# Performance work log

Measured on AMD Instinct MI355X. Metric: run time of the kernel, lower is better.

Reference implementation:

```python
import jax, jax.numpy as jnp
import numpy as np

B, S, D, H = 2, 2048, 2048, 16
HD = D // H  # head_dim = 128


def setup_inputs() -> dict:
    key = jax.random.key(0)
    ks = jax.random.split(key, 5)
    scale = 1.0 / np.sqrt(D)
    return {
        "x": jax.random.normal(ks[0], (B, S, D), dtype=jnp.float32),
        "wq": jax.random.normal(ks[1], (D, D), dtype=jnp.float32) * scale,
        "wk": jax.random.normal(ks[2], (D, D), dtype=jnp.float32) * scale,
        "wv": jax.random.normal(ks[3], (D, D), dtype=jnp.float32) * scale,
        "wo": jax.random.normal(ks[4], (D, D), dtype=jnp.float32) * scale,
        "bo": jnp.zeros((D,), dtype=jnp.float32),
    }


def reference(x, wq, wk, wv, wo, bo):
    b, s, _ = x.shape
    # torch Linear: y = x @ W.T ; then view(b,s,H,HD) and transpose to (b,H,s,HD)
    q = (x @ wq.T).reshape(b, s, H, HD).transpose(0, 2, 1, 3)
    k = (x @ wk.T).reshape(b, s, H, HD).transpose(0, 2, 1, 3)
    v = (x @ wv.T).reshape(b, s, H, HD).transpose(0, 2, 1, 3)
    scores = jnp.einsum("bhqd,bhkd->bhqk", q, k)
    causal = jnp.triu(jnp.ones((s, s), dtype=bool), k=1)  # True above diagonal
    scores = jnp.where(causal[None, None], -jnp.inf, scores)
    attn = jax.nn.softmax(scores / np.sqrt(HD), axis=-1)
    # dropout p=0.0 -> identity
    ctx = jnp.einsum("bhqk,bhkd->bhqd", attn, v)
    ctx = ctx.transpose(0, 2, 1, 3).reshape(b, s, D)
    return ctx @ wo.T + bo
```

## Files before the change

### kernel.cpp

```cpp
#include <hip/hip_runtime.h>
#include <math.h>

typedef __bf16 bf16_t;
typedef __bf16 bf16x8 __attribute__((ext_vector_type(8)));
typedef float f32x4 __attribute__((ext_vector_type(4)));
typedef float f32x16 __attribute__((ext_vector_type(16)));

__device__ __forceinline__ void gload_lds16(const bf16_t* g, bf16_t* l) {
    __builtin_amdgcn_global_load_lds((const __attribute__((address_space(1))) void*)g,
                                     (__attribute__((address_space(3))) void*)l, 16, 0, 0);
}

__global__ __launch_bounds__(256) void cvt_all(const float* __restrict__ x,
                                               const float* __restrict__ wq,
                                               const float* __restrict__ wk,
                                               const float* __restrict__ wv,
                                               const float* __restrict__ wo,
                                               bf16_t* __restrict__ dst) {
    int c = blockIdx.x * 256 + threadIdx.x;
    const float* src;
    size_t off;
    if (c < 1048576) { src = x; off = c; }
    else {
        int q = (c - 1048576) >> 19;
        src = (q == 0) ? wq : (q == 1) ? wk : (q == 2) ? wv : wo;
        off = (c - 1048576) & 524287;
    }
    const float4* p = (const float4*)src + off * 2;
    float4 a = p[0], b = p[1];
    union { bf16_t h[8]; uint4 u; } pk;
    pk.h[0] = (bf16_t)a.x; pk.h[1] = (bf16_t)a.y; pk.h[2] = (bf16_t)a.z; pk.h[3] = (bf16_t)a.w;
    pk.h[4] = (bf16_t)b.x; pk.h[5] = (bf16_t)b.y; pk.h[6] = (bf16_t)b.z; pk.h[7] = (bf16_t)b.w;
    ((uint4*)dst)[c] = pk.u;
}

template <int MODE, typename OutT>
__device__ __forceinline__ void gemm_core(bf16_t* __restrict__ AsB, bf16_t* __restrict__ BsB,
                                          const bf16_t* __restrict__ A,
                                          const bf16_t* __restrict__ Bm,
                                          const float* __restrict__ bias,
                                          OutT* __restrict__ C, bf16_t* __restrict__ Vt,
                                          int M, int N, int K, int bx, int by) {
    const int tid = threadIdx.x;
    const int w = tid >> 6, l = tid & 63;
    const int l16 = l & 15, lg = l >> 4;
    const int wr = w >> 1, wc = w & 1;
    const int m0 = bx * 256, n0 = by * 128;
    const int lsw = l16 & 7;

    f32x4 acc[4][4] = {};

    auto stageA = [&](int k0, int buf) {
#pragma unroll
        for (int j = 0; j < 4; ++j) {
            int c = tid + j * 512;
            int row = c >> 3;
            int kc = (c & 7) ^ (row & 7);
            gload_lds16(A + (size_t)(m0 + row) * K + k0 + kc * 8,
                        &AsB[buf * 16384 + (j * 512 + w * 64) * 8]);
        }
    };
    auto stageB = [&](int k0, int buf) {
#pragma unroll
        for (int j = 0; j < 2; ++j) {
            int c = tid + j * 512;
            int row = c >> 3;
            int kc = (c & 7) ^ (row & 7);
            gload_lds16(Bm + (size_t)(n0 + row) * K + k0 + kc * 8,
                        &BsB[buf * 8192 + (j * 512 + w * 64) * 8]);
        }
    };

    stageA(0, 0); stageB(0, 0);
    stageA(64, 1); stageB(64, 1);
    asm volatile("s_waitcnt vmcnt(6)" ::: "memory");
    __builtin_amdgcn_s_barrier();

    const int nt = K / 64;
    int cur = 0;
    for (int t = 0; t < nt; ++t) {
        int nxt = cur + 2; if (nxt >= 3) nxt -= 3;
        const bool pf = (t + 2 < nt);
        const int k2 = (t + 2) * 64;
        const bf16_t* Asc = &AsB[cur * 16384];
        const bf16_t* Bsc = &BsB[cur * 8192];

        if (pf) { stageA(k2, nxt); stageB(k2, nxt); }

        bf16x8 af[4][2], bfr[4][2];
#pragma unroll
        for (int mf = 0; mf < 4; ++mf)
#pragma unroll
            for (int ks = 0; ks < 2; ++ks) {
                int arow = wr * 64 + mf * 16 + l16;
                af[mf][ks] = *(const bf16x8*)&Asc[arow * 64 + (((ks << 2) | lg) ^ lsw) * 8];
            }
#pragma unroll
        for (int nf = 0; nf < 4; ++nf)
#pragma unroll
            for (int ks = 0; ks < 2; ++ks) {
                int brow = wc * 64 + nf * 16 + l16;
                bfr[nf][ks] = *(const bf16x8*)&Bsc[brow * 64 + (((ks << 2) | lg) ^ lsw) * 8];
            }
#pragma unroll
        for (int ks = 0; ks < 2; ++ks)
#pragma unroll
            for (int mf = 0; mf < 4; ++mf)
#pragma unroll
                for (int nf = 0; nf < 4; ++nf)
                    acc[mf][nf] = __builtin_amdgcn_mfma_f32_16x16x32_bf16(af[mf][ks], bfr[nf][ks], acc[mf][nf], 0, 0, 0);

        if (pf) asm volatile("s_waitcnt vmcnt(6)" ::: "memory");
        else    asm volatile("s_waitcnt vmcnt(0)" ::: "memory");
        __builtin_amdgcn_s_barrier();
        cur = (cur + 1 == 3) ? 0 : cur + 1;
    }

    if constexpr (MODE == 2) {
#pragma unroll
        for (int mf = 0; mf < 4; ++mf)
#pragma unroll
            for (int nf = 0; nf < 4; ++nf) {
                int col = n0 + wc * 64 + nf * 16 + l16;
                int hh = col >> 7, dh = col & 127;
                int rowbase = m0 + wr * 64 + mf * 16 + lg * 4;
                int bb = rowbase >> 11, s = rowbase & 2047;
                union { bf16_t h[4]; ushort4 u4; } pk;
#pragma unroll
                for (int r = 0; r < 4; ++r) pk.h[r] = (bf16_t)acc[mf][nf][r];
                *(ushort4*)&Vt[(((size_t)(bb * 16 + hh)) * 128 + dh) * 2048 + s] = pk.u4;
            }
    } else {
#pragma unroll
        for (int mf = 0; mf < 4; ++mf)
#pragma unroll
            for (int nf = 0; nf < 4; ++nf) {
                int col = n0 + wc * 64 + nf * 16 + l16;
                float bv = (MODE == 1) ? bias[col] : 0.f;
#pragma unroll
                for (int r = 0; r < 4; ++r) {
                    int row = m0 + wr * 64 + mf * 16 + lg * 4 + r;
                    C[(size_t)row * N + col] = (OutT)(acc[mf][nf][r] + bv);
                }
            }
    }
}

__global__ __launch_bounds__(512, 2) void gemm_qkv(const bf16_t* __restrict__ A,
                                                   const bf16_t* __restrict__ W0,
                                                   const bf16_t* __restrict__ W1,
                                                   const bf16_t* __restrict__ W2,
                                                   bf16_t* __restrict__ O0, bf16_t* __restrict__ O1,
                                                   bf16_t* __restrict__ Vt, int M, int N, int K) {
    __shared__ __align__(16) bf16_t As[3 * 256 * 64];
    __shared__ __align__(16) bf16_t Bs[3 * 128 * 64];
    int flat = blockIdx.x + 16 * (blockIdx.y + 16 * blockIdx.z);
    int idx = (flat & 7) * 96 + (flat >> 3);
    int bx = idx & 15, by = (idx >> 4) & 15, bz = idx >> 8;
    if (bz == 0)      gemm_core<0, bf16_t>(As, Bs, A, W0, nullptr, O0, nullptr, M, N, K, bx, by);
    else if (bz == 1) gemm_core<0, bf16_t>(As, Bs, A, W1, nullptr, O1, nullptr, M, N, K, bx, by);
    else              gemm_core<2, bf16_t>(As, Bs, A, W2, nullptr, (bf16_t*)nullptr, Vt, M, N, K, bx, by);
}

__global__ __launch_bounds__(512, 2) void gemm_bias_f32(const bf16_t* __restrict__ A,
                                                        const bf16_t* __restrict__ Bm,
                                                        const float* __restrict__ bias,
                                                        float* __restrict__ C, int M, int N, int K) {
    __shared__ __align__(16) bf16_t As[3 * 256 * 64];
    __shared__ __align__(16) bf16_t Bs[3 * 128 * 64];
    int flat = blockIdx.x + 16 * blockIdx.y;
    int idx = (flat & 7) * 32 + (flat >> 3);
    int bx = idx & 15, by = idx >> 4;
    gemm_core<1, float>(As, Bs, A, Bm, bias, C, nullptr, M, N, K, bx, by);
}

__global__ __launch_bounds__(512, 2) void attn_fwd(const bf16_t* __restrict__ Q,
                                                   const bf16_t* __restrict__ Kk,
                                                   const bf16_t* __restrict__ Vt,
                                                   bf16_t* __restrict__ Ctx, int S, int H) {
    const int D = H * 128;
    const int bh = blockIdx.x;
    const int qb = blockIdx.y;
    const int b = bh >> 4, h = bh & 15;
    const int tid = threadIdx.x;
    const int w = tid >> 6, l = tid & 63;
    const int l32 = l & 31, hi = l >> 5;
    const int q0w = qb * 256 + w * 32;
    const int qrow = q0w + l32;

    __shared__ __align__(16) bf16_t ks[2][64 * 128];
    __shared__ __align__(16) bf16_t vs[2][128 * 64];

    bf16x8 qf[8];
    {
        const bf16_t* qp = Q + (size_t)(b * S + qrow) * D + h * 128 + hi * 8;
#pragma unroll
        for (int d = 0; d < 8; ++d) qf[d] = *(const bf16x8*)(qp + d * 16);
    }

    f32x16 ctx[4] = {};
    float mrun = -INFINITY, lrun = 0.f;
    const float Cs = 0.08838834764831845f * 1.4426950408889634f;

    auto stage = [&](int k0, int buf) {
#pragma unroll
        for (int j = 0; j < 2; ++j) {
            int c = tid + j * 512;
            int r = c >> 4;
            int c16 = (c & 15) ^ (r & 7);
            gload_lds16(Kk + (size_t)(b * S + k0 + r) * D + h * 128 + c16 * 8,
                        &ks[buf][(j * 512 + w * 64) * 8]);
            int dd = c >> 3;
            int k8 = (c & 7) ^ (dd & 7);
            gload_lds16(Vt + ((size_t)bh * 128 + dd) * S + k0 + k8 * 8,
                        &vs[buf][(j * 512 + w * 64) * 8]);
        }
    };

    stage(0, 0);
    const int nkt = 4 * qb + 4;
    int cur = 0;
    for (int kt = 0; kt < nkt; ++kt) {
        __syncthreads();
        if (kt + 1 < nkt) stage((kt + 1) * 64, cur ^ 1);
        const int k0 = kt * 64;
        if (k0 <= q0w + 31) {
            f32x16 sacc[2] = {};
#pragma unroll
            for (int d = 0; d < 8; ++d) {
#pragma unroll
                for (int t2 = 0; t2 < 2; ++t2) {
                    int row = t2 * 32 + l32;
                    int c16 = (2 * d + hi) ^ (row & 7);
                    bf16x8 kf = *(const bf16x8*)&ks[cur][(row * 16 + c16) * 8];
                    sacc[t2] = __builtin_amdgcn_mfma_f32_32x32x16_bf16(kf, qf[d], sacc[t2], 0, 0, 0);
                }
            }
            const bool diag = (k0 + 63 > q0w);
#pragma unroll
            for (int t2 = 0; t2 < 2; ++t2)
#pragma unroll
                for (int c = 0; c < 16; ++c) {
                    float s = sacc[t2][c] * Cs;
                    if (diag) {
                        int key = k0 + 32 * t2 + (c & 3) + 8 * (c >> 2) + 4 * hi;
                        if (key > qrow) s = -INFINITY;
                    }
                    sacc[t2][c] = s;
                }
            float tm[16];
#pragma unroll
            for (int c = 0; c < 16; ++c) tm[c] = fmaxf(sacc[0][c], sacc[1][c]);
#pragma unroll
            for (int sft = 8; sft; sft >>= 1)
#pragma unroll
                for (int c = 0; c < 8; ++c)
                    if (c < sft) tm[c] = fmaxf(tm[c], tm[c + sft]);
            float pmax = fmaxf(tm[0], __shfl_xor(tm[0], 32));
            if (!__all(pmax <= mrun + 8.f)) {
                float mnew = fmaxf(mrun, pmax);
                float alpha = exp2f(mrun - mnew);
                lrun *= alpha;
#pragma unroll
                for (int dblk = 0; dblk < 4; ++dblk)
#pragma unroll
                    for (int c = 0; c < 16; ++c) ctx[dblk][c] *= alpha;
                mrun = mnew;
            }
#pragma unroll
            for (int t2 = 0; t2 < 2; ++t2)
#pragma unroll
                for (int c = 0; c < 16; ++c) sacc[t2][c] = exp2f(sacc[t2][c] - mrun);
            float ts[16];
#pragma unroll
            for (int c = 0; c < 16; ++c) ts[c] = sacc[0][c] + sacc[1][c];
#pragma unroll
            for (int sft = 8; sft; sft >>= 1)
#pragma unroll
                for (int c = 0; c < 8; ++c)
                    if (c < sft) ts[c] += ts[c + sft];
            lrun += ts[0] + __shfl_xor(ts[0], 32);
            bf16x8 pa[4];
#pragma unroll
            for (int ksx = 0; ksx < 4; ++ksx) {
                const int t2 = ksx >> 1, cb = (ksx & 1) * 8;
                union { bf16_t hh[4]; unsigned u[2]; } Wlo, Whi;
#pragma unroll
                for (int i = 0; i < 4; ++i) {
                    Wlo.hh[i] = (bf16_t)sacc[t2][cb + i];
                    Whi.hh[i] = (bf16_t)sacc[t2][cb + 4 + i];
                }
                unsigned s0 = hi ? Wlo.u[0] : Whi.u[0];
                unsigned s1 = hi ? Wlo.u[1] : Whi.u[1];
                unsigned r0 = __shfl_xor(s0, 32);
                unsigned r1 = __shfl_xor(s1, 32);
                union { unsigned u[4]; bf16x8 v; } F;
                if (hi == 0) { F.u[0] = Wlo.u[0]; F.u[1] = Wlo.u[1]; F.u[2] = r0; F.u[3] = r1; }
                else         { F.u[0] = r0; F.u[1] = r1; F.u[2] = Whi.u[0]; F.u[3] = Whi.u[1]; }
                pa[ksx] = F.v;
            }
#pragma unroll
            for (int ksx = 0; ksx < 4; ++ksx)
#pragma unroll
                for (int dblk = 0; dblk < 4; ++dblk) {
                    int dd = dblk * 32 + l32;
                    int k8 = (2 * ksx + hi) ^ (dd & 7);
                    bf16x8 vf = *(const bf16x8*)&vs[cur][(dd * 8 + k8) * 8];
                    ctx[dblk] = __builtin_amdgcn_mfma_f32_32x32x16_bf16(vf, pa[ksx], ctx[dblk], 0, 0, 0);
                }
        }
        cur ^= 1;
    }
    float invl = 1.f / lrun;
    bf16_t* op = Ctx + (size_t)(b * S + qrow) * D + h * 128;
#pragma unroll
    for (int dblk = 0; dblk < 4; ++dblk)
#pragma unroll
        for (int cg = 0; cg < 4; ++cg) {
            union { bf16_t hh[4]; ushort4 u4; } pk;
#pragma unroll
            for (int i = 0; i < 4; ++i) pk.hh[i] = (bf16_t)(ctx[dblk][cg * 4 + i] * invl);
            *(ushort4*)&op[dblk * 32 + cg * 8 + hi * 4] = pk.u4;
        }
}

extern "C" void kernel_launch(void* const* d_in, const int* in_sizes, int n_in,
                              void* d_out, int out_size, void* d_ws, size_t ws_size,
                              hipStream_t stream) {
    const int B = 2, S = 2048, D = 2048, H = 16;
    const int M = B * S;
    const float* x  = (const float*)d_in[0];
    const float* wq = (const float*)d_in[1];
    const float* wk = (const float*)d_in[2];
    const float* wv = (const float*)d_in[3];
    const float* wo = (const float*)d_in[4];
    const float* bo = (const float*)d_in[5];
    float* out = (float*)d_out;

    char* ws = (char*)d_ws;
    const size_t MB = 1024 * 1024;
    if (ws_size < 128 * MB) return;
    bf16_t* xb  = (bf16_t*)(ws);
    bf16_t* wqb = (bf16_t*)(ws + 16 * MB);
    bf16_t* wkb = (bf16_t*)(ws + 24 * MB);
    bf16_t* wvb = (bf16_t*)(ws + 32 * MB);
    bf16_t* wob = (bf16_t*)(ws + 40 * MB);
    bf16_t* qb  = (bf16_t*)(ws + 48 * MB);
    bf16_t* kb  = (bf16_t*)(ws + 64 * MB);
    bf16_t* vtb = (bf16_t*)(ws + 80 * MB);
    bf16_t* cxb = (bf16_t*)(ws + 96 * MB);

    cvt_all<<<12288, 256, 0, stream>>>(x, wq, wk, wv, wo, xb);
    gemm_qkv<<<dim3(16, 16, 3), 512, 0, stream>>>(xb, wqb, wkb, wvb, qb, kb, vtb, M, D, D);
    attn_fwd<<<dim3(32, 8), 512, 0, stream>>>(qb, kb, vtb, cxb, S, H);
    gemm_bias_f32<<<dim3(16, 16), 512, 0, stream>>>(cxb, wob, bo, out, M, D, D);
}
```

Measured before the change: 312.0 us.

## Halve GEMM K-tile for higher occupancy and split attention into smaller query tiles

After: 258.0 us. -17.3%, faster.

```diff
diff --git a/kernel.cpp b/kernel.cpp
--- a/kernel.cpp
+++ b/kernel.cpp
@@ -46,71 +46,63 @@
     const int l16 = l & 15, lg = l >> 4;
     const int wr = w >> 1, wc = w & 1;
     const int m0 = bx * 256, n0 = by * 128;
-    const int lsw = l16 & 7;
 
     f32x4 acc[4][4] = {};
 
     auto stageA = [&](int k0, int buf) {
 #pragma unroll
-        for (int j = 0; j < 4; ++j) {
+        for (int j = 0; j < 2; ++j) {
             int c = tid + j * 512;
-            int row = c >> 3;
-            int kc = (c & 7) ^ (row & 7);
+            int row = c >> 2;
+            int kc = (c & 3) ^ ((row >> 1) & 3);
             gload_lds16(A + (size_t)(m0 + row) * K + k0 + kc * 8,
-                        &AsB[buf * 16384 + (j * 512 + w * 64) * 8]);
+                        &AsB[buf * 8192 + (j * 512 + w * 64) * 8]);
         }
     };
     auto stageB = [&](int k0, int buf) {
-#pragma unroll
-        for (int j = 0; j < 2; ++j) {
-            int c = tid + j * 512;
-            int row = c >> 3;
-            int kc = (c & 7) ^ (row & 7);
-            gload_lds16(Bm + (size_t)(n0 + row) * K + k0 + kc * 8,
-                        &BsB[buf * 8192 + (j * 512 + w * 64) * 8]);
-        }
+        int row = tid >> 2;
+        int kc = (tid & 3) ^ ((row >> 1) & 3);
+        gload_lds16(Bm + (size_t)(n0 + row) * K + k0 + kc * 8,
+                    &BsB[buf * 4096 + (w * 64) * 8]);
     };
 
     stageA(0, 0); stageB(0, 0);
-    stageA(64, 1); stageB(64, 1);
-    asm volatile("s_waitcnt vmcnt(6)" ::: "memory");
+    stageA(32, 1); stageB(32, 1);
+    asm volatile("s_waitcnt vmcnt(3)" ::: "memory");
     __builtin_amdgcn_s_barrier();
 
-    const int nt = K / 64;
+    const int nt = K / 32;
     int cur = 0;
     for (int t = 0; t < nt; ++t) {
         int nxt = cur + 2; if (nxt >= 3) nxt -= 3;
         const bool pf = (t + 2 < nt);
-        const int k2 = (t + 2) * 64;
-        const bf16_t* Asc = &AsB[cur * 16384];
-        const bf16_t* Bsc = &BsB[cur * 8192];
-
+        const int k2 = (t + 2) * 32;
+        const bf16_t* Asc = &AsB[cur * 8192];
+        const bf16_t* Bsc = &BsB[cur * 4096];
+
+        bf16x8 af[4], bfr[4];
+#pragma unroll
+        for (int mf = 0; mf < 4; ++mf) {
+            int arow = wr * 64 + mf * 16 + l16;
+            af[mf] = *(const bf16x8*)&Asc[arow * 32 + (lg ^ ((arow >> 1) & 3)) * 8];
+        }
+#pragma unroll
+        for (int nf = 0; nf < 4; ++nf) {
+            int brow = wc * 64 + nf * 16 + l16;
+            bfr[nf] = *(const bf16x8*)&Bsc[brow * 32 + (lg ^ ((brow >> 1) & 3)) * 8];
+        }
         if (pf) { stageA(k2, nxt); stageB(k2, nxt); }
-
-        bf16x8 af[4][2], bfr[4][2];
+        asm volatile("s_waitcnt lgkmcnt(0)" ::: "memory");
+        __builtin_amdgcn_sched_barrier(0);
+        __builtin_amdgcn_s_setprio(1);
 #pragma unroll
         for (int mf = 0; mf < 4; ++mf)
 #pragma unroll
-            for (int ks = 0; ks < 2; ++ks) {
-                int arow = wr * 64 + mf * 16 + l16;
-                af[mf][ks] = *(const bf16x8*)&Asc[arow * 64 + (((ks << 2) | lg) ^ lsw) * 8];
-            }
-#pragma unroll
-        for (int nf = 0; nf < 4; ++nf)
-#pragma unroll
-            for (int ks = 0; ks < 2; ++ks) {
-                int brow = wc * 64 + nf * 16 + l16;
-                bfr[nf][ks] = *(const bf16x8*)&Bsc[brow * 64 + (((ks << 2) | lg) ^ lsw) * 8];
-            }
-#pragma unroll
-        for (int ks = 0; ks < 2; ++ks)
-#pragma unroll
-            for (int mf = 0; mf < 4; ++mf)
-#pragma unroll
-                for (int nf = 0; nf < 4; ++nf)
-                    acc[mf][nf] = __builtin_amdgcn_mfma_f32_16x16x32_bf16(af[mf][ks], bfr[nf][ks], acc[mf][nf], 0, 0, 0);
-
-        if (pf) asm volatile("s_waitcnt vmcnt(6)" ::: "memory");
+            for (int nf = 0; nf < 4; ++nf)
+                acc[mf][nf] = __builtin_amdgcn_mfma_f32_16x16x32_bf16(af[mf], bfr[nf], acc[mf][nf], 0, 0, 0);
+        __builtin_amdgcn_s_setprio(0);
+
+        if (pf) asm volatile("s_waitcnt vmcnt(3)" ::: "memory");
         else    asm volatile("s_waitcnt vmcnt(0)" ::: "memory");
         __builtin_amdgcn_s_barrier();
         cur = (cur + 1 == 3) ? 0 : cur + 1;
@@ -146,14 +138,14 @@
     }
 }
 
-__global__ __launch_bounds__(512, 2) void gemm_qkv(const bf16_t* __restrict__ A,
+__global__ __launch_bounds__(512, 4) void gemm_qkv(const bf16_t* __restrict__ A,
                                                    const bf16_t* __restrict__ W0,
                                                    const bf16_t* __restrict__ W1,
                                                    const bf16_t* __restrict__ W2,
                                                    bf16_t* __restrict__ O0, bf16_t* __restrict__ O1,
                                                    bf16_t* __restrict__ Vt, int M, int N, int K) {
-    __shared__ __align__(16) bf16_t As[3 * 256 * 64];
-    __shared__ __align__(16) bf16_t Bs[3 * 128 * 64];
+    __shared__ __align__(16) bf16_t As[3 * 256 * 32];
+    __shared__ __align__(16) bf16_t Bs[3 * 128 * 32];
     int flat = blockIdx.x + 16 * (blockIdx.y + 16 * blockIdx.z);
     int idx = (flat & 7) * 96 + (flat >> 3);
     int bx = idx & 15, by = (idx >> 4) & 15, bz = idx >> 8;
@@ -162,30 +154,31 @@
     else              gemm_core<2, bf16_t>(As, Bs, A, W2, nullptr, (bf16_t*)nullptr, Vt, M, N, K, bx, by);
 }
 
-__global__ __launch_bounds__(512, 2) void gemm_bias_f32(const bf16_t* __restrict__ A,
+__global__ __launch_bounds__(512, 4) void gemm_bias_f32(const bf16_t* __restrict__ A,
                                                         const bf16_t* __restrict__ Bm,
                                                         const float* __restrict__ bias,
                                                         float* __restrict__ C, int M, int N, int K) {
-    __shared__ __align__(16) bf16_t As[3 * 256 * 64];
-    __shared__ __align__(16) bf16_t Bs[3 * 128 * 64];
+    __shared__ __align__(16) bf16_t As[3 * 256 * 32];
+    __shared__ __align__(16) bf16_t Bs[3 * 128 * 32];
     int flat = blockIdx.x + 16 * blockIdx.y;
     int idx = (flat & 7) * 32 + (flat >> 3);
     int bx = idx & 15, by = idx >> 4;
     gemm_core<1, float>(As, Bs, A, Bm, bias, C, nullptr, M, N, K, bx, by);
 }
 
-__global__ __launch_bounds__(512, 2) void attn_fwd(const bf16_t* __restrict__ Q,
+__global__ __launch_bounds__(256, 2) void attn_fwd(const bf16_t* __restrict__ Q,
                                                    const bf16_t* __restrict__ Kk,
                                                    const bf16_t* __restrict__ Vt,
                                                    bf16_t* __restrict__ Ctx, int S, int H) {
     const int D = H * 128;
     const int bh = blockIdx.x;
-    const int qb = blockIdx.y;
+    const int y = blockIdx.y;
+    const int qt = (y < 8) ? (15 - y) : (y - 8);
     const int b = bh >> 4, h = bh & 15;
     const int tid = threadIdx.x;
     const int w = tid >> 6, l = tid & 63;
     const int l32 = l & 31, hi = l >> 5;
-    const int q0w = qb * 256 + w * 32;
+    const int q0w = qt * 128 + w * 32;
     const int qrow = q0w + l32;
 
     __shared__ __align__(16) bf16_t ks[2][64 * 128];
@@ -204,21 +197,21 @@
 
     auto stage = [&](int k0, int buf) {
 #pragma unroll
-        for (int j = 0; j < 2; ++j) {
-            int c = tid + j * 512;
+        for (int j = 0; j < 4; ++j) {
+            int c = tid + j * 256;
             int r = c >> 4;
             int c16 = (c & 15) ^ (r & 7);
             gload_lds16(Kk + (size_t)(b * S + k0 + r) * D + h * 128 + c16 * 8,
-                        &ks[buf][(j * 512 + w * 64) * 8]);
+                        &ks[buf][(j * 256 + w * 64) * 8]);
             int dd = c >> 3;
             int k8 = (c & 7) ^ (dd & 7);
             gload_lds16(Vt + ((size_t)bh * 128 + dd) * S + k0 + k8 * 8,
-                        &vs[buf][(j * 512 + w * 64) * 8]);
+                        &vs[buf][(j * 256 + w * 64) * 8]);
         }
     };
 
     stage(0, 0);
-    const int nkt = 4 * qb + 4;
+    const int nkt = 2 * qt + 2;
     int cur = 0;
     for (int kt = 0; kt < nkt; ++kt) {
         __syncthreads();
@@ -352,6 +345,6 @@
 
     cvt_all<<<12288, 256, 0, stream>>>(x, wq, wk, wv, wo, xb);
     gemm_qkv<<<dim3(16, 16, 3), 512, 0, stream>>>(xb, wqb, wkb, wvb, qb, kb, vtb, M, D, D);
-    attn_fwd<<<dim3(32, 8), 512, 0, stream>>>(qb, kb, vtb, cxb, S, H);
+    attn_fwd<<<dim3(32, 16), 256, 0, stream>>>(qb, kb, vtb, cxb, S, H);
     gemm_bias_f32<<<dim3(16, 16), 512, 0, stream>>>(cxb, wob, bo, out, M, D, D);
 }
```
